# Kernel tuning notes

Hardware: AMD Instinct MI355X
Metric: run time of the kernel (lower is better)

The kernel has to match this reference:

```python
import jax, jax.numpy as jnp
import numpy as np

DIMS = 4

def mlp(x, W1, b1, W2, b2, W3, b3, Wo, bo):
    # x: (4,) -> scalar log(g_rr)
    h = jnp.tanh(x @ W1 + b1)
    h = jnp.tanh(h @ W2 + b2)
    h = jnp.tanh(h @ W3 + b3)
    return (h @ Wo + bo)[0]

def metric(x, params):
    # build_g: spherical metric with learned g_rr = exp(net(x))
    g_rr = jnp.exp(mlp(x, *params))
    r, th = x[1], x[2]
    diag = jnp.stack([-jnp.ones(()), g_rr, r ** 2, (r * jnp.sin(th)) ** 2])
    return jnp.diag(diag)  # (4,4)

def christoffel(x, params):
    g = metric(x, params)
    dg = jax.jacfwd(lambda xx: metric(xx, params))(x)  # dg[i,j,k] = d g_ij / d x^k
    g_inv = jnp.linalg.inv(g)
    # Gamma^a_bc = 0.5 g^{ad} (d_c g_db + d_b g_dc - d_d g_bc)
    sym = dg + jnp.transpose(dg, (0, 2, 1)) - jnp.transpose(dg, (2, 0, 1))
    gamma = 0.5 * jnp.einsum('ad,dbc->abc', g_inv, sym)
    return gamma, g_inv

def einstein_per_sample(x, params):
    gamma, g_inv = christoffel(x, params)
    # D[a,i,j,k] = d_k Gamma^a_ij (second nested forward-mode jacobian)
    D = jax.jacfwd(lambda xx: christoffel(xx, params)[0])(x)
    # R^a_bcd = d_c Gamma^a_db - d_d Gamma^a_cb + G^a_ce G^e_db - G^a_de G^e_cb
    riemann = (jnp.einsum('adbc->abcd', D) - jnp.einsum('acbd->abcd', D)
               + jnp.einsum('ace,edb->abcd', gamma, gamma)
               - jnp.einsum('ade,ecb->abcd', gamma, gamma))
    ricci = jnp.einsum('abad->bd', riemann)
    ricci_scalar = jnp.einsum('bd,bd->', g_inv, ricci)
    ricci_up = jnp.einsum('ac,bd,cd->ab', g_inv, g_inv, ricci)
    return ricci_up - 0.5 * g_inv * ricci_scalar  # contravariant Einstein tensor


def setup_inputs() -> dict:
    key = jax.random.key(0)
    ks = jax.random.split(key, 5)
    B, H = 8192, 256
    # coords in a well-conditioned region (avoid r ~ 0 which makes g singular)
    coords = jax.random.uniform(ks[0], (B, DIMS), dtype=jnp.float32) * 0.9 + 0.1
    def w(k, shape):
        fan_in = shape[0]
        return jax.random.normal(k, shape, dtype=jnp.float32) / np.sqrt(fan_in)
    return {
        'coords': coords,
        'W1': w(ks[1], (DIMS, H)), 'b1': jnp.zeros((H,), jnp.float32),
        'W2': w(ks[2], (H, H)),   'b2': jnp.zeros((H,), jnp.float32),
        'W3': w(ks[3], (H, H)),   'b3': jnp.zeros((H,), jnp.float32),
        'Wo': w(ks[4], (H, 1)),   'bo': jnp.zeros((1,), jnp.float32),
    }


def reference(coords, W1, b1, W2, b2, W3, b3, Wo, bo):
    params = (W1, b1, W2, b2, W3, b3, Wo, bo)
    # Batched Einstein tensor G^{ab}(x) for every sample: (B, 4, 4)
    return jax.vmap(lambda x: einstein_per_sample(x, params))(coords)
```

## Files before the change

kernel.cpp:

```cpp
#include <hip/hip_runtime.h>
#include <math.h>

typedef _Float16 half8 __attribute__((ext_vector_type(8)));
typedef float floatx4 __attribute__((ext_vector_type(4)));

#define HDIM 256
#define NC 15
#define NCP 16
#define SPB 8
#define MR 128
#define NWAVE 4
#define NT 4


__device__ __forceinline__ void einstein_tail(
    float f, const float* Gf, const float* Hs, float r, float th,
    float* __restrict__ outp)
{
    float Hf[4][4];
    {
        int qq = 0;
#pragma unroll
        for (int k = 0; k < 4; ++k)
#pragma unroll
            for (int l = k; l < 4; ++l) { Hf[k][l] = Hs[qq]; Hf[l][k] = Hs[qq]; ++qq; }
    }
    float sn = sinf(th), cs = cosf(th);
    float E  = expf(f);

    float gd[4] = {-1.f, E, r * r, r * r * sn * sn};
    float gi[4];
#pragma unroll
    for (int a = 0; a < 4; ++a) gi[a] = 1.f / gd[a];

    float dgv[4][4];
    float ddg[4][4][4];
#pragma unroll
    for (int a = 0; a < 4; ++a)
#pragma unroll
        for (int k = 0; k < 4; ++k) {
            dgv[a][k] = 0.f;
#pragma unroll
            for (int l = 0; l < 4; ++l) ddg[a][k][l] = 0.f;
        }
#pragma unroll
    for (int k = 0; k < 4; ++k) dgv[1][k] = E * Gf[k];
    dgv[2][1] = 2.f * r;
    dgv[3][1] = 2.f * r * sn * sn;
    dgv[3][2] = 2.f * r * r * sn * cs;
#pragma unroll
    for (int k = 0; k < 4; ++k)
#pragma unroll
        for (int l = 0; l < 4; ++l)
            ddg[1][k][l] = E * fmaf(Gf[k], Gf[l], Hf[k][l]);
    ddg[2][1][1] = 2.f;
    ddg[3][1][1] = 2.f * sn * sn;
    ddg[3][1][2] = 4.f * r * sn * cs;
    ddg[3][2][1] = 4.f * r * sn * cs;
    ddg[3][2][2] = 2.f * r * r * (cs * cs - sn * sn);

    auto SYMF = [&](int a, int i, int jx) -> float {
        float sy = 0.f;
        if (a == i)  sy += dgv[a][jx];
        if (a == jx) sy += dgv[a][i];
        if (i == jx) sy -= dgv[i][a];
        return sy;
    };
    auto DF = [&](int a, int i, int jx, int k) -> float {
        float ds = 0.f;
        if (a == i)  ds += ddg[a][jx][k];
        if (a == jx) ds += ddg[a][i][k];
        if (i == jx) ds -= ddg[i][a][k];
        return 0.5f * (gi[a] * ds - gi[a] * gi[a] * dgv[a][k] * SYMF(a, i, jx));
    };

    float Gm[4][4][4];
#pragma unroll
    for (int a = 0; a < 4; ++a)
#pragma unroll
        for (int i = 0; i < 4; ++i)
#pragma unroll
            for (int jx = 0; jx < 4; ++jx)
                Gm[a][i][jx] = 0.5f * gi[a] * SYMF(a, i, jx);

    float ric[4][4];
#pragma unroll
    for (int b = 0; b < 4; ++b)
#pragma unroll
        for (int d = 0; d < 4; ++d) {
            float sum = 0.f;
#pragma unroll
            for (int a = 0; a < 4; ++a) {
                sum += DF(a, d, b, a) - DF(a, a, b, d);
#pragma unroll
                for (int e = 0; e < 4; ++e)
                    sum += Gm[a][a][e] * Gm[e][d][b] - Gm[a][d][e] * Gm[e][a][b];
            }
            ric[b][d] = sum;
        }

    float Rs = 0.f;
#pragma unroll
    for (int b = 0; b < 4; ++b) Rs += gi[b] * ric[b][b];

#pragma unroll
    for (int a = 0; a < 4; ++a)
#pragma unroll
        for (int b = 0; b < 4; ++b) {
            float v = gi[a] * gi[b] * ric[a][b];
            if (a == b) v -= 0.5f * gi[a] * Rs;
            outp[a * 4 + b] = v;
        }
}

__global__ __launch_bounds__(256) void pack_wt(
    const float* __restrict__ W2, const float* __restrict__ W3,
    _Float16* __restrict__ Wt)
{
    __shared__ float t[64][65];
    const int m    = blockIdx.x >> 4;
    const float* W = m ? W3 : W2;
    const int tile = blockIdx.x & 15;
    const int k0 = (tile >> 2) * 64, j0 = (tile & 3) * 64;
    const int tx = threadIdx.x & 63, ty = threadIdx.x >> 6;
#pragma unroll
    for (int i = 0; i < 16; ++i) {
        int k = ty + i * 4;
        t[k][tx] = W[(k0 + k) * HDIM + j0 + tx];
    }
    __syncthreads();
#pragma unroll
    for (int i = 0; i < 16; ++i) {
        int jj = ty + i * 4;
        Wt[(size_t)m * HDIM * HDIM + (j0 + jj) * HDIM + k0 + tx] =
            (_Float16)t[tx][jj];
    }
}

template <bool TW>
__global__ __launch_bounds__(256, 2) void mlp_fused(
    const float* __restrict__ coords,
    const float* __restrict__ W1, const float* __restrict__ b1,
    const float* __restrict__ W2, const float* __restrict__ b2,
    const float* __restrict__ W3, const float* __restrict__ b3,
    const float* __restrict__ Wo, const float* __restrict__ bo,
    const _Float16* __restrict__ Wt,
    float* __restrict__ out, int B)
{
    __shared__ __align__(16) _Float16 st[MR * HDIM];

    const int tid  = threadIdx.x;
    const int w    = tid >> 6;
    const int lane = tid & 63;
    const int col  = lane & 15;
    const int q    = lane >> 4;
    const int s0   = blockIdx.x * SPB;

    floatx4 acc[8][NT];

    auto f4get = [](const float4& v, int i) -> float {
        switch (i & 3) { case 0: return v.x; case 1: return v.y;
                         case 2: return v.z; default: return v.w; }
    };

    auto produce1 = [&]() {
        const int sl = tid & 7;
        const int tc = tid >> 3;
        int ss = s0 + sl; if (ss >= B) ss = B - 1;
        const float x0 = coords[ss * 4 + 0];
        const float x1 = coords[ss * 4 + 1];
        const float x2 = coords[ss * 4 + 2];
        const float x3 = coords[ss * 4 + 3];
        const int jg = tc * 8;
        float4 wa[4][2];
#pragma unroll
        for (int k = 0; k < 4; ++k) {
            wa[k][0] = *(const float4*)&W1[k * HDIM + jg];
            wa[k][1] = *(const float4*)&W1[k * HDIM + jg + 4];
        }
        float4 bb0 = *(const float4*)&b1[jg];
        float4 bb1 = *(const float4*)&b1[jg + 4];
        half8 ch[NCP];
#pragma unroll
        for (int jj = 0; jj < 8; ++jj) ch[15][jj] = (_Float16)0.f;
#pragma unroll
        for (int jj = 0; jj < 8; ++jj) {
            const int h = jj >> 2;
            float w0 = f4get(wa[0][h], jj), w1 = f4get(wa[1][h], jj);
            float w2v = f4get(wa[2][h], jj), w3v = f4get(wa[3][h], jj);
            float a = f4get(h ? bb1 : bb0, jj);
            a = fmaf(x0, w0, a); a = fmaf(x1, w1, a);
            a = fmaf(x2, w2v, a); a = fmaf(x3, w3v, a);
            float v = tanhf(a), tp = 1.f - v * v, m2 = -2.f * v * tp;
            float g[4] = {w0, w1, w2v, w3v};
            ch[0][jj] = (_Float16)v;
#pragma unroll
            for (int k = 0; k < 4; ++k) ch[1 + k][jj] = (_Float16)(tp * g[k]);
            int idx = 5;
#pragma unroll
            for (int aa = 0; aa < 4; ++aa)
#pragma unroll
                for (int bb2 = aa; bb2 < 4; ++bb2) {
                    ch[idx][jj] = (_Float16)(m2 * g[aa] * g[bb2]); ++idx;
                }
        }
#pragma unroll
        for (int c = 0; c < NCP; ++c) {
            const int m = 16 * (c >> 1) + 4 * (sl >> 1) + 2 * (sl & 1) + (c & 1);
            const int addr = m * HDIM + (((tc ^ m) & 31) << 3);
            *(half8*)&st[addr] = ch[c];
        }
    };

    auto init_acc = [&](const float* __restrict__ b) {
#pragma unroll
        for (int nt = 0; nt < NT; ++nt) {
            float bj = b[w * 64 + nt * 16 + col];
#pragma unroll
            for (int mt = 0; mt < 8; ++mt)
#pragma unroll
                for (int r = 0; r < 4; ++r) acc[mt][nt][r] = 0.f;
            acc[0][nt][0] = bj;
            acc[0][nt][2] = bj;
        }
    };

    auto gemm_full = [&](const float* __restrict__ W, int layer) {
#pragma unroll
        for (int ks = 0; ks < 8; ++ks) {
            const int kg = ks * 32 + q * 8;
            half8 bf[NT];
#pragma unroll
            for (int nt = 0; nt < NT; ++nt) {
                const int j = w * 64 + nt * 16 + col;
                if constexpr (TW) {
                    bf[nt] = *(const half8*)&Wt[((size_t)layer * HDIM + j) * HDIM + kg];
                } else {
#pragma unroll
                    for (int i = 0; i < 8; ++i)
                        bf[nt][i] = (_Float16)W[(kg + i) * HDIM + j];
                }
            }
            const int lc = ks * 4 + q;
#pragma unroll
            for (int mt = 0; mt < 8; ++mt) {
                const int m = 16 * mt + col;
                half8 af = *(const half8*)&st[m * HDIM + (((lc ^ m) & 31) << 3)];
#pragma unroll
                for (int nt = 0; nt < NT; ++nt)
                    acc[mt][nt] = __builtin_amdgcn_mfma_f32_16x16x32_f16(
                        af, bf[nt], acc[mt][nt], 0, 0, 0);
            }
        }
    };

    auto transform_store = [&]() {
#pragma unroll
        for (int nt = 0; nt < NT; ++nt) {
            const int j = w * 64 + nt * 16 + col;
            const int jc = j >> 3, jb = j & 7;
#pragma unroll
            for (int sv = 0; sv < 2; ++sv) {
                float pre[NCP];
#pragma unroll
                for (int c = 0; c < NCP; ++c)
                    pre[c] = acc[c >> 1][nt][sv * 2 + (c & 1)];
                float v = tanhf(pre[0]), tp = 1.f - v * v, m2 = -2.f * v * tp;
                float g[4] = {pre[1], pre[2], pre[3], pre[4]};
                float ns[NCP];
                ns[0] = v;
#pragma unroll
                for (int k = 0; k < 4; ++k) ns[1 + k] = tp * g[k];
                int idx = 5;
#pragma unroll
                for (int aa = 0; aa < 4; ++aa)
#pragma unroll
                    for (int bb2 = aa; bb2 < 4; ++bb2) {
                        ns[idx] = fmaf(tp, pre[idx], m2 * g[aa] * g[bb2]); ++idx;
                    }
                ns[15] = 0.f;
#pragma unroll
                for (int c = 0; c < NCP; ++c) {
                    const int m = 16 * (c >> 1) + 4 * q + 2 * sv + (c & 1);
                    st[m * HDIM + (((jc ^ m) & 31) << 3) + jb] = (_Float16)ns[c];
                }
            }
        }
    };

    produce1();
    __syncthreads();
    init_acc(b2);
    gemm_full(W2, 0);
    __syncthreads();
    transform_store();
    __syncthreads();
    init_acc(b3);
    gemm_full(W3, 1);

    __syncthreads();
    float* part = (float*)st;
    float* fin  = ((float*)st) + 512;
    float wo[NT];
#pragma unroll
    for (int nt = 0; nt < NT; ++nt) wo[nt] = Wo[w * 64 + nt * 16 + col];

    float on2[2][NC];
#pragma unroll
    for (int sv = 0; sv < 2; ++sv)
#pragma unroll
        for (int c = 0; c < NC; ++c) on2[sv][c] = 0.f;
#pragma unroll
    for (int nt = 0; nt < NT; ++nt)
#pragma unroll
        for (int sv = 0; sv < 2; ++sv) {
            float pre[NCP];
#pragma unroll
            for (int c = 0; c < NCP; ++c)
                pre[c] = acc[c >> 1][nt][sv * 2 + (c & 1)];
            float v = tanhf(pre[0]), tp = 1.f - v * v, m2 = -2.f * v * tp;
            float g[4] = {pre[1], pre[2], pre[3], pre[4]};
            on2[sv][0] = fmaf(wo[nt], v, on2[sv][0]);
#pragma unroll
            for (int k = 0; k < 4; ++k)
                on2[sv][1 + k] = fmaf(wo[nt], tp * g[k], on2[sv][1 + k]);
            int idx = 5;
#pragma unroll
            for (int aa = 0; aa < 4; ++aa)
#pragma unroll
                for (int bb2 = aa; bb2 < 4; ++bb2) {
                    on2[sv][idx] = fmaf(wo[nt],
                        fmaf(tp, pre[idx], m2 * g[aa] * g[bb2]), on2[sv][idx]);
                    ++idx;
                }
        }
#pragma unroll
    for (int mask = 1; mask < 16; mask <<= 1)
#pragma unroll
        for (int sv = 0; sv < 2; ++sv)
#pragma unroll
            for (int c = 0; c < NC; ++c)
                on2[sv][c] += __shfl_xor(on2[sv][c], mask, 64);
    if (col == 0) {
#pragma unroll
        for (int sv = 0; sv < 2; ++sv)
#pragma unroll
            for (int c = 0; c < NC; ++c)
                part[(w * SPB + 2 * q + sv) * NC + c] = on2[sv][c];
    }
    __syncthreads();
    if (tid < SPB * NC) {
        const int sl = tid / NC, c = tid % NC;
        float v = 0.f;
#pragma unroll
        for (int ww = 0; ww < NWAVE; ++ww) v += part[(ww * SPB + sl) * NC + c];
        if (c == 0) v += bo[0];
        fin[sl * 16 + c] = v;
    }
    __syncthreads();
    if (tid < SPB) {
        int s = s0 + tid;
        if (s < B) {
            float f = fin[tid * 16 + 0];
            float Gf[4], Hs[10];
#pragma unroll
            for (int k = 0; k < 4; ++k) Gf[k] = fin[tid * 16 + 1 + k];
#pragma unroll
            for (int qq = 0; qq < 10; ++qq) Hs[qq] = fin[tid * 16 + 5 + qq];
            float r  = coords[s * 4 + 1];
            float th = coords[s * 4 + 2];
            float res[16];
            einstein_tail(f, Gf, Hs, r, th, res);
#pragma unroll
            for (int e = 0; e < 16; ++e) out[s * 16 + e] = res[e];
        }
    }
}

extern "C" void kernel_launch(void* const* d_in, const int* in_sizes, int n_in,
                              void* d_out, int out_size, void* d_ws, size_t ws_size,
                              hipStream_t stream) {
    const float* coords = (const float*)d_in[0];
    const float* W1 = (const float*)d_in[1];
    const float* b1 = (const float*)d_in[2];
    const float* W2 = (const float*)d_in[3];
    const float* b2 = (const float*)d_in[4];
    const float* W3 = (const float*)d_in[5];
    const float* b3 = (const float*)d_in[6];
    const float* Wo = (const float*)d_in[7];
    const float* bo = (const float*)d_in[8];
    float* out = (float*)d_out;
    const int B = in_sizes[0] / 4;
    const int nblocks = (B + SPB - 1) / SPB;

    const size_t wt_bytes = (size_t)2 * HDIM * HDIM * sizeof(_Float16);
    if (ws_size >= wt_bytes) {
        _Float16* Wt = (_Float16*)d_ws;
        pack_wt<<<32, 256, 0, stream>>>(W2, W3, Wt);
        mlp_fused<true><<<nblocks, 256, 0, stream>>>(
            coords, W1, b1, W2, b2, W3, b3, Wo, bo, Wt, out, B);
    } else {
        mlp_fused<false><<<nblocks, 256, 0, stream>>>(
            coords, W1, b1, W2, b2, W3, b3, Wo, bo, nullptr, out, B);
    }
}
```

Baseline: 133.6 us.

## Halve samples per block to raise occupancy and use fast tanh approximation

```diff
diff --git a/kernel.cpp b/kernel.cpp
--- a/kernel.cpp
+++ b/kernel.cpp
@@ -2,16 +2,22 @@
 #include <math.h>
 
 typedef _Float16 half8 __attribute__((ext_vector_type(8)));
+typedef _Float16 half4 __attribute__((ext_vector_type(4)));
 typedef float floatx4 __attribute__((ext_vector_type(4)));
 
 #define HDIM 256
 #define NC 15
 #define NCP 16
-#define SPB 8
-#define MR 128
+#define SPB 4
+#define MR 64
 #define NWAVE 4
 #define NT 4
 
+
+__device__ __forceinline__ float ftanh(float x) {
+    float e = __expf(2.f * x);
+    return fmaf(-2.f, __builtin_amdgcn_rcpf(e + 1.f), 1.f);
+}
 
 __device__ __forceinline__ void einstein_tail(
     float f, const float* Gf, const float* Hs, float r, float th,
@@ -138,7 +144,7 @@
 }
 
 template <bool TW>
-__global__ __launch_bounds__(256, 2) void mlp_fused(
+__global__ __launch_bounds__(256, 4) void mlp_fused(
     const float* __restrict__ coords,
     const float* __restrict__ W1, const float* __restrict__ b1,
     const float* __restrict__ W2, const float* __restrict__ b2,
@@ -156,7 +162,7 @@
     const int q    = lane >> 4;
     const int s0   = blockIdx.x * SPB;
 
-    floatx4 acc[8][NT];
+    floatx4 acc[4][NT];
 
     auto f4get = [](const float4& v, int i) -> float {
         switch (i & 3) { case 0: return v.x; case 1: return v.y;
@@ -164,34 +170,30 @@
     };
 
     auto produce1 = [&]() {
-        const int sl = tid & 7;
-        const int tc = tid >> 3;
+        const int sl = tid & 3;
+        const int tc = tid >> 2;
         int ss = s0 + sl; if (ss >= B) ss = B - 1;
         const float x0 = coords[ss * 4 + 0];
         const float x1 = coords[ss * 4 + 1];
         const float x2 = coords[ss * 4 + 2];
         const float x3 = coords[ss * 4 + 3];
-        const int jg = tc * 8;
-        float4 wa[4][2];
-#pragma unroll
-        for (int k = 0; k < 4; ++k) {
-            wa[k][0] = *(const float4*)&W1[k * HDIM + jg];
-            wa[k][1] = *(const float4*)&W1[k * HDIM + jg + 4];
-        }
-        float4 bb0 = *(const float4*)&b1[jg];
-        float4 bb1 = *(const float4*)&b1[jg + 4];
-        half8 ch[NCP];
-#pragma unroll
-        for (int jj = 0; jj < 8; ++jj) ch[15][jj] = (_Float16)0.f;
-#pragma unroll
-        for (int jj = 0; jj < 8; ++jj) {
-            const int h = jj >> 2;
-            float w0 = f4get(wa[0][h], jj), w1 = f4get(wa[1][h], jj);
-            float w2v = f4get(wa[2][h], jj), w3v = f4get(wa[3][h], jj);
-            float a = f4get(h ? bb1 : bb0, jj);
+        const int jg = tc * 4;
+        float4 wa[4];
+#pragma unroll
+        for (int k = 0; k < 4; ++k)
+            wa[k] = *(const float4*)&W1[k * HDIM + jg];
+        float4 bb = *(const float4*)&b1[jg];
+        half4 ch[NCP];
+#pragma unroll
+        for (int jj = 0; jj < 4; ++jj) ch[15][jj] = (_Float16)0.f;
+#pragma unroll
+        for (int jj = 0; jj < 4; ++jj) {
+            float w0 = f4get(wa[0], jj), w1 = f4get(wa[1], jj);
+            float w2v = f4get(wa[2], jj), w3v = f4get(wa[3], jj);
+            float a = f4get(bb, jj);
             a = fmaf(x0, w0, a); a = fmaf(x1, w1, a);
             a = fmaf(x2, w2v, a); a = fmaf(x3, w3v, a);
-            float v = tanhf(a), tp = 1.f - v * v, m2 = -2.f * v * tp;
+            float v = ftanh(a), tp = 1.f - v * v, m2 = -2.f * v * tp;
             float g[4] = {w0, w1, w2v, w3v};
             ch[0][jj] = (_Float16)v;
 #pragma unroll
@@ -206,9 +208,10 @@
         }
 #pragma unroll
         for (int c = 0; c < NCP; ++c) {
-            const int m = 16 * (c >> 1) + 4 * (sl >> 1) + 2 * (sl & 1) + (c & 1);
-            const int addr = m * HDIM + (((tc ^ m) & 31) << 3);
-            *(half8*)&st[addr] = ch[c];
+            const int m = 16 * (c >> 2) + 4 * sl + (c & 3);
+            const int addr = m * HDIM + ((((tc >> 1) ^ m) & 31) << 3)
+                           + ((tc & 1) << 2);
+            *(half4*)&st[addr] = ch[c];
         }
     };
 
@@ -217,11 +220,10 @@
         for (int nt = 0; nt < NT; ++nt) {
             float bj = b[w * 64 + nt * 16 + col];
 #pragma unroll
-            for (int mt = 0; mt < 8; ++mt)
+            for (int mt = 0; mt < 4; ++mt)
 #pragma unroll
                 for (int r = 0; r < 4; ++r) acc[mt][nt][r] = 0.f;
             acc[0][nt][0] = bj;
-            acc[0][nt][2] = bj;
         }
     };
 
@@ -243,7 +245,7 @@
             }
             const int lc = ks * 4 + q;
 #pragma unroll
-            for (int mt = 0; mt < 8; ++mt) {
+            for (int mt = 0; mt < 4; ++mt) {
                 const int m = 16 * mt + col;
                 half8 af = *(const half8*)&st[m * HDIM + (((lc ^ m) & 31) << 3)];
 #pragma unroll
@@ -259,31 +261,28 @@
         for (int nt = 0; nt < NT; ++nt) {
             const int j = w * 64 + nt * 16 + col;
             const int jc = j >> 3, jb = j & 7;
-#pragma unroll
-            for (int sv = 0; sv < 2; ++sv) {
-                float pre[NCP];
-#pragma unroll
-                for (int c = 0; c < NCP; ++c)
-                    pre[c] = acc[c >> 1][nt][sv * 2 + (c & 1)];
-                float v = tanhf(pre[0]), tp = 1.f - v * v, m2 = -2.f * v * tp;
-                float g[4] = {pre[1], pre[2], pre[3], pre[4]};
-                float ns[NCP];
-                ns[0] = v;
-#pragma unroll
-                for (int k = 0; k < 4; ++k) ns[1 + k] = tp * g[k];
-                int idx = 5;
-#pragma unroll
-                for (int aa = 0; aa < 4; ++aa)
-#pragma unroll
-                    for (int bb2 = aa; bb2 < 4; ++bb2) {
-                        ns[idx] = fmaf(tp, pre[idx], m2 * g[aa] * g[bb2]); ++idx;
-                    }
-                ns[15] = 0.f;
-#pragma unroll
-                for (int c = 0; c < NCP; ++c) {
-                    const int m = 16 * (c >> 1) + 4 * q + 2 * sv + (c & 1);
-                    st[m * HDIM + (((jc ^ m) & 31) << 3) + jb] = (_Float16)ns[c];
+            float pre[NCP];
+#pragma unroll
+            for (int c = 0; c < NCP; ++c)
+                pre[c] = acc[c >> 2][nt][c & 3];
+            float v = ftanh(pre[0]), tp = 1.f - v * v, m2 = -2.f * v * tp;
+            float g[4] = {pre[1], pre[2], pre[3], pre[4]};
+            float ns[NCP];
+            ns[0] = v;
+#pragma unroll
+            for (int k = 0; k < 4; ++k) ns[1 + k] = tp * g[k];
+            int idx = 5;
+#pragma unroll
+            for (int aa = 0; aa < 4; ++aa)
+#pragma unroll
+                for (int bb2 = aa; bb2 < 4; ++bb2) {
+                    ns[idx] = fmaf(tp, pre[idx], m2 * g[aa] * g[bb2]); ++idx;
                 }
+            ns[15] = 0.f;
+#pragma unroll
+            for (int c = 0; c < NCP; ++c) {
+                const int m = 16 * (c >> 2) + 4 * q + (c & 3);
+                st[m * HDIM + (((jc ^ m) & 31) << 3) + jb] = (_Float16)ns[c];
             }
         }
     };
@@ -300,53 +299,45 @@
 
     __syncthreads();
     float* part = (float*)st;
-    float* fin  = ((float*)st) + 512;
+    float* fin  = ((float*)st) + 256;
     float wo[NT];
 #pragma unroll
     for (int nt = 0; nt < NT; ++nt) wo[nt] = Wo[w * 64 + nt * 16 + col];
 
-    float on2[2][NC];
-#pragma unroll
-    for (int sv = 0; sv < 2; ++sv)
-#pragma unroll
-        for (int c = 0; c < NC; ++c) on2[sv][c] = 0.f;
-#pragma unroll
-    for (int nt = 0; nt < NT; ++nt)
-#pragma unroll
-        for (int sv = 0; sv < 2; ++sv) {
-            float pre[NCP];
-#pragma unroll
-            for (int c = 0; c < NCP; ++c)
-                pre[c] = acc[c >> 1][nt][sv * 2 + (c & 1)];
-            float v = tanhf(pre[0]), tp = 1.f - v * v, m2 = -2.f * v * tp;
-            float g[4] = {pre[1], pre[2], pre[3], pre[4]};
-            on2[sv][0] = fmaf(wo[nt], v, on2[sv][0]);
-#pragma unroll
-            for (int k = 0; k < 4; ++k)
-                on2[sv][1 + k] = fmaf(wo[nt], tp * g[k], on2[sv][1 + k]);
-            int idx = 5;
-#pragma unroll
-            for (int aa = 0; aa < 4; ++aa)
-#pragma unroll
-                for (int bb2 = aa; bb2 < 4; ++bb2) {
-                    on2[sv][idx] = fmaf(wo[nt],
-                        fmaf(tp, pre[idx], m2 * g[aa] * g[bb2]), on2[sv][idx]);
-                    ++idx;
-                }
-        }
+    float on[NC];
+#pragma unroll
+    for (int c = 0; c < NC; ++c) on[c] = 0.f;
+#pragma unroll
+    for (int nt = 0; nt < NT; ++nt) {
+        float pre[NCP];
+#pragma unroll
+        for (int c = 0; c < NCP; ++c)
+            pre[c] = acc[c >> 2][nt][c & 3];
+        float v = ftanh(pre[0]), tp = 1.f - v * v, m2 = -2.f * v * tp;
+        float g[4] = {pre[1], pre[2], pre[3], pre[4]};
+        on[0] = fmaf(wo[nt], v, on[0]);
+#pragma unroll
+        for (int k = 0; k < 4; ++k)
+            on[1 + k] = fmaf(wo[nt], tp * g[k], on[1 + k]);
+        int idx = 5;
+#pragma unroll
+        for (int aa = 0; aa < 4; ++aa)
+#pragma unroll
+            for (int bb2 = aa; bb2 < 4; ++bb2) {
+                on[idx] = fmaf(wo[nt],
+                    fmaf(tp, pre[idx], m2 * g[aa] * g[bb2]), on[idx]);
+                ++idx;
+            }
+    }
 #pragma unroll
     for (int mask = 1; mask < 16; mask <<= 1)
 #pragma unroll
-        for (int sv = 0; sv < 2; ++sv)
-#pragma unroll
-            for (int c = 0; c < NC; ++c)
-                on2[sv][c] += __shfl_xor(on2[sv][c], mask, 64);
+        for (int c = 0; c < NC; ++c)
+            on[c] += __shfl_xor(on[c], mask, 64);
     if (col == 0) {
 #pragma unroll
-        for (int sv = 0; sv < 2; ++sv)
-#pragma unroll
-            for (int c = 0; c < NC; ++c)
-                part[(w * SPB + 2 * q + sv) * NC + c] = on2[sv][c];
+        for (int c = 0; c < NC; ++c)
+            part[(w * SPB + q) * NC + c] = on[c];
     }
     __syncthreads();
     if (tid < SPB * NC) {
```

After: 151.1 us. +13.1%, slower.

## Split Einstein tail into separate kernel and use fast exp-based tanh

Applied to the files above, without the earlier changes.

```diff
diff --git a/kernel.cpp b/kernel.cpp
--- a/kernel.cpp
+++ b/kernel.cpp
@@ -13,6 +13,11 @@
 #define NT 4
 
 
+__device__ __forceinline__ float ftanh(float x) {
+    float e = __expf(2.f * x);
+    return fmaf(-2.f, __builtin_amdgcn_rcpf(e + 1.f), 1.f);
+}
+
 __device__ __forceinline__ void einstein_tail(
     float f, const float* Gf, const float* Hs, float r, float th,
     float* __restrict__ outp)
@@ -111,6 +116,29 @@
             if (a == b) v -= 0.5f * gi[a] * Rs;
             outp[a * 4 + b] = v;
         }
+}
+
+__global__ __launch_bounds__(64) void einstein_k(
+    const float* __restrict__ coords, const float* __restrict__ fin,
+    float* __restrict__ out, int B)
+{
+    const int s = blockIdx.x * 64 + threadIdx.x;
+    if (s >= B) return;
+    float4 f0 = *(const float4*)&fin[s * 16 + 0];
+    float4 f1 = *(const float4*)&fin[s * 16 + 4];
+    float4 f2 = *(const float4*)&fin[s * 16 + 8];
+    float4 f3 = *(const float4*)&fin[s * 16 + 12];
+    float f = f0.x;
+    float Gf[4] = {f0.y, f0.z, f0.w, f1.x};
+    float Hs[10] = {f1.y, f1.z, f1.w, f2.x, f2.y, f2.z, f2.w, f3.x, f3.y, f3.z};
+    float r  = coords[s * 4 + 1];
+    float th = coords[s * 4 + 2];
+    float res[16];
+    einstein_tail(f, Gf, Hs, r, th, res);
+#pragma unroll
+    for (int e = 0; e < 4; ++e)
+        *(float4*)&out[s * 16 + e * 4] =
+            make_float4(res[e*4+0], res[e*4+1], res[e*4+2], res[e*4+3]);
 }
 
 __global__ __launch_bounds__(256) void pack_wt(
@@ -137,7 +165,7 @@
     }
 }
 
-template <bool TW>
+template <bool TW, bool SPLIT>
 __global__ __launch_bounds__(256, 2) void mlp_fused(
     const float* __restrict__ coords,
     const float* __restrict__ W1, const float* __restrict__ b1,
@@ -145,6 +173,7 @@
     const float* __restrict__ W3, const float* __restrict__ b3,
     const float* __restrict__ Wo, const float* __restrict__ bo,
     const _Float16* __restrict__ Wt,
+    float* __restrict__ finbuf,
     float* __restrict__ out, int B)
 {
     __shared__ __align__(16) _Float16 st[MR * HDIM];
@@ -191,7 +220,7 @@
             float a = f4get(h ? bb1 : bb0, jj);
             a = fmaf(x0, w0, a); a = fmaf(x1, w1, a);
             a = fmaf(x2, w2v, a); a = fmaf(x3, w3v, a);
-            float v = tanhf(a), tp = 1.f - v * v, m2 = -2.f * v * tp;
+            float v = ftanh(a), tp = 1.f - v * v, m2 = -2.f * v * tp;
             float g[4] = {w0, w1, w2v, w3v};
             ch[0][jj] = (_Float16)v;
 #pragma unroll
@@ -265,7 +294,7 @@
 #pragma unroll
                 for (int c = 0; c < NCP; ++c)
                     pre[c] = acc[c >> 1][nt][sv * 2 + (c & 1)];
-                float v = tanhf(pre[0]), tp = 1.f - v * v, m2 = -2.f * v * tp;
+                float v = ftanh(pre[0]), tp = 1.f - v * v, m2 = -2.f * v * tp;
                 float g[4] = {pre[1], pre[2], pre[3], pre[4]};
                 float ns[NCP];
                 ns[0] = v;
@@ -318,7 +347,7 @@
 #pragma unroll
             for (int c = 0; c < NCP; ++c)
                 pre[c] = acc[c >> 1][nt][sv * 2 + (c & 1)];
-            float v = tanhf(pre[0]), tp = 1.f - v * v, m2 = -2.f * v * tp;
+            float v = ftanh(pre[0]), tp = 1.f - v * v, m2 = -2.f * v * tp;
             float g[4] = {pre[1], pre[2], pre[3], pre[4]};
             on2[sv][0] = fmaf(wo[nt], v, on2[sv][0]);
 #pragma unroll
@@ -355,24 +384,31 @@
 #pragma unroll
         for (int ww = 0; ww < NWAVE; ++ww) v += part[(ww * SPB + sl) * NC + c];
         if (c == 0) v += bo[0];
-        fin[sl * 16 + c] = v;
-    }
-    __syncthreads();
-    if (tid < SPB) {
-        int s = s0 + tid;
-        if (s < B) {
-            float f = fin[tid * 16 + 0];
-            float Gf[4], Hs[10];
-#pragma unroll
-            for (int k = 0; k < 4; ++k) Gf[k] = fin[tid * 16 + 1 + k];
-#pragma unroll
-            for (int qq = 0; qq < 10; ++qq) Hs[qq] = fin[tid * 16 + 5 + qq];
-            float r  = coords[s * 4 + 1];
-            float th = coords[s * 4 + 2];
-            float res[16];
-            einstein_tail(f, Gf, Hs, r, th, res);
-#pragma unroll
-            for (int e = 0; e < 16; ++e) out[s * 16 + e] = res[e];
+        if constexpr (SPLIT) {
+            int s = s0 + sl;
+            if (s < B) finbuf[s * 16 + c] = v;
+        } else {
+            fin[sl * 16 + c] = v;
+        }
+    }
+    if constexpr (!SPLIT) {
+        __syncthreads();
+        if (tid < SPB) {
+            int s = s0 + tid;
+            if (s < B) {
+                float f = fin[tid * 16 + 0];
+                float Gf[4], Hs[10];
+#pragma unroll
+                for (int k = 0; k < 4; ++k) Gf[k] = fin[tid * 16 + 1 + k];
+#pragma unroll
+                for (int qq = 0; qq < 10; ++qq) Hs[qq] = fin[tid * 16 + 5 + qq];
+                float r  = coords[s * 4 + 1];
+                float th = coords[s * 4 + 2];
+                float res[16];
+                einstein_tail(f, Gf, Hs, r, th, res);
+#pragma unroll
+                for (int e = 0; e < 16; ++e) out[s * 16 + e] = res[e];
+            }
         }
     }
 }
@@ -393,14 +429,23 @@
     const int B = in_sizes[0] / 4;
     const int nblocks = (B + SPB - 1) / SPB;
 
-    const size_t wt_bytes = (size_t)2 * HDIM * HDIM * sizeof(_Float16);
-    if (ws_size >= wt_bytes) {
+    const size_t wt_bytes  = (size_t)2 * HDIM * HDIM * sizeof(_Float16);
+    const size_t fin_bytes = (size_t)B * 16 * sizeof(float);
+
+    if (ws_size >= wt_bytes + fin_bytes) {
+        _Float16* Wt = (_Float16*)d_ws;
+        float* finbuf = (float*)((char*)d_ws + wt_bytes);
+        pack_wt<<<32, 256, 0, stream>>>(W2, W3, Wt);
+        mlp_fused<true, true><<<nblocks, 256, 0, stream>>>(
+            coords, W1, b1, W2, b2, W3, b3, Wo, bo, Wt, finbuf, out, B);
+        einstein_k<<<(B + 63) / 64, 64, 0, stream>>>(coords, finbuf, out, B);
+    } else if (ws_size >= wt_bytes) {
         _Float16* Wt = (_Float16*)d_ws;
         pack_wt<<<32, 256, 0, stream>>>(W2, W3, Wt);
-        mlp_fused<true><<<nblocks, 256, 0, stream>>>(
-            coords, W1, b1, W2, b2, W3, b3, Wo, bo, Wt, out, B);
+        mlp_fused<true, false><<<nblocks, 256, 0, stream>>>(
+            coords, W1, b1, W2, b2, W3, b3, Wo, bo, Wt, nullptr, out, B);
     } else {
-        mlp_fused<false><<<nblocks, 256, 0, stream>>>(
-            coords, W1, b1, W2, b2, W3, b3, Wo, bo, nullptr, out, B);
-    }
-}
+        mlp_fused<false, false><<<nblocks, 256, 0, stream>>>(
+            coords, W1, b1, W2, b2, W3, b3, Wo, bo, nullptr, nullptr, out, B);
+    }
+}
```

After: 126.7 us. 5.2% less time.
